# Performance work log

Measured on AMD Instinct MI355X. Metric: run time of the kernel, lower is better.

The kernel has to match this reference:

```python
import jax, jax.numpy as jnp
import numpy as np

B, S, D = 1, 2048, 1024
H, HD = 16, 64            # attn_num, head dim (D = H*HD)
TE, K, ED = 16, 2, 512    # experts, top_k, expert_dim
DS = 2048                 # shared_expert_dim
EPS = 1e-5
THETA = 10000.0
RSF = 1.0                 # routed_scaling_factor


def rmsnorm(x, w):
    return x * jax.lax.rsqrt(jnp.mean(x * x, axis=-1, keepdims=True) + EPS) * w


def rope(x):
    # x: [B,H,S,a]; half-split rotary as in RotaryEmb
    a = x.shape[-1]
    inv = (1.0 / THETA) ** (jnp.arange(0, a, 2, dtype=jnp.float32) / a)
    fr = jnp.outer(jnp.arange(x.shape[2], dtype=jnp.float32), inv)[None, None]  # [1,1,S,a/2]
    c, s = jnp.cos(fr), jnp.sin(fr)
    x1, x2 = jnp.split(x, 2, axis=-1)
    return jnp.concatenate([x1 * c + x2 * s, -x1 * s + x2 * c], axis=-1)


def setup_inputs() -> dict:
    key = jax.random.key(0)
    ks = jax.random.split(key, 16)
    w = 0.02
    return {
        "x_input": jax.random.normal(ks[0], (B, S, D), jnp.float32),
        "indices": jax.random.randint(ks[1], (B * S, K), 0, TE),
        "values": jax.random.normal(ks[2], (B * S, K), jnp.float32),
        "attn_w": jax.random.normal(ks[3], (3 * D, D), jnp.float32) * w,
        "attn_o_w": jax.random.normal(ks[4], (D, D), jnp.float32) * w,
        "attn_norm_w": jnp.ones((D,), jnp.float32),
        "ffn_norm_w": jnp.ones((D,), jnp.float32),
        "ffn_experts": jax.random.normal(ks[5], (3, TE, D, ED), jnp.float32) * w,
        "main_keys": jax.random.normal(ks[6], (D, TE), jnp.float32) * w,
        "main_bias": jnp.zeros((TE,), jnp.float32),
        "output_coeff": jnp.ones((1, 1, D), jnp.float32),
        "ffn_up_w": jax.random.normal(ks[7], (2 * DS, D), jnp.float32) * w,
        "ffn_down_w": jax.random.normal(ks[8], (D, DS), jnp.float32) * w,
        "shared_norm_w": jnp.ones((D,), jnp.float32),
    }


def reference(x_input, indices, values, attn_w, attn_o_w, attn_norm_w, ffn_norm_w,
              ffn_experts, main_keys, main_bias, output_coeff, ffn_up_w,
              ffn_down_w, shared_norm_w):
    # --- attention block ---
    x = rmsnorm(x_input, attn_norm_w)
    qkv = x @ attn_w.T                                  # [B,S,3D]
    xq, xk, xv = jnp.split(qkv, 3, axis=-1)
    def heads(t):
        return t.reshape(B, S, H, HD).transpose(0, 2, 1, 3)  # [B,H,S,HD]
    q, k, v = rope(heads(xq)), rope(heads(xk)), heads(xv)
    att = jnp.einsum('bhqa,bhka->bhqk', q, k) / jnp.sqrt(jnp.float32(HD))
    causal = jnp.tril(jnp.ones((S, S), bool))
    att = jnp.where(causal, att, jnp.finfo(att.dtype).min)
    att = jax.nn.softmax(att, axis=-1)
    o = jnp.einsum('bhqk,bhka->bhqa', att, v)
    x_attn = o.transpose(0, 2, 1, 3).reshape(B, S, D)
    x_ffn_input = x_attn @ attn_o_w.T + x_input

    # --- router ---
    x_ffn = rmsnorm(x_ffn_input, ffn_norm_w)
    T = B * S
    token_values = (x_ffn @ main_keys).reshape(T, TE)
    tv = jnp.take_along_axis(token_values, indices, axis=-1)  # [T,K]
    vals = values + tv + main_bias[indices]
    scores = jax.nn.softmax(vals, axis=-1) * RSF              # [T,K]

    # --- grouped GEMM experts (SwiGLU), dense combine over experts ---
    combine = jnp.zeros((T, TE), x_ffn.dtype).at[
        jnp.arange(T)[:, None], indices].add(scores)          # [T,TE]
    xf = x_ffn.reshape(T, D)
    h1 = jnp.einsum('td,edh->eth', xf, ffn_experts[0])
    h2 = jnp.einsum('td,edh->eth', xf, ffn_experts[1])
    g = jax.nn.silu(h1) * h2                                  # [TE,T,ED]
    ye = jnp.einsum('eth,edh->etd', g, ffn_experts[2])        # [TE,T,D]
    y = jnp.einsum('etd,te->td', ye, combine).reshape(B, S, D)
    y = y * output_coeff

    # --- shared SwiGLU expert ---
    x1, x2 = jnp.split(x_ffn @ ffn_up_w.T, 2, axis=-1)
    y_shared = (jax.nn.silu(x1) * x2) @ ffn_down_w.T
    y_shared = rmsnorm(y_shared, shared_norm_w)

    return y + y_shared + x_ffn_input
```

## Files before the change

kernel.cpp:

```cpp
#include <hip/hip_runtime.h>
#include <hip/hip_bf16.h>

using bf16 = __hip_bfloat16;

#define S_   2048
#define D_   1024
#define H_   16
#define HD_  64
#define TE_  16
#define ED_  512
#define DS_  2048
#define CAP_ 512

#define NEG_ -1e30f

typedef __attribute__((ext_vector_type(8))) short bf16x8;
typedef __attribute__((ext_vector_type(4))) short bf16x4;
typedef __attribute__((ext_vector_type(4))) float f32x4;
#define MFMA16(a, b, c) __builtin_amdgcn_mfma_f32_16x16x32_bf16(a, b, c, 0, 0, 0)

__device__ __forceinline__ void storeF(float* p, float v) { *p = v; }
__device__ __forceinline__ void storeF(bf16* p, float v)  { *p = __float2bfloat16(v); }
__device__ __forceinline__ short cvt1(float f) {
    bf16 h = __float2bfloat16(f);
    return *(short*)&h;
}
__device__ __forceinline__ float b2f(short s) {
    return __uint_as_float(((unsigned)(unsigned short)s) << 16);
}

__device__ __forceinline__ void load16(const bf16* g, short* l) {
    __builtin_amdgcn_global_load_lds(
        (const __attribute__((address_space(1))) unsigned*)g,
        (__attribute__((address_space(3))) unsigned*)l, 16, 0, 0);
}

__global__ __launch_bounds__(256) void convert_kernel(
        const float* __restrict__ src, bf16* __restrict__ dst)
{
    const size_t i = ((size_t)blockIdx.x*256 + threadIdx.x)*8;
    const float4 f0 = *(const float4*)(src + i);
    const float4 f1 = *(const float4*)(src + i + 4);
    short t8[8];
    t8[0]=cvt1(f0.x); t8[1]=cvt1(f0.y); t8[2]=cvt1(f0.z); t8[3]=cvt1(f0.w);
    t8[4]=cvt1(f1.x); t8[5]=cvt1(f1.y); t8[6]=cvt1(f1.z); t8[7]=cvt1(f1.w);
    *(bf16x8*)(dst + i) = *(bf16x8*)t8;
}

__global__ __launch_bounds__(256) void mkT_kernel(
        const float* __restrict__ mk, float* __restrict__ mkT)
{
    const int idx = blockIdx.x*256 + threadIdx.x;
    const int e = idx >> 10, d = idx & 1023;
    mkT[idx] = mk[d*TE_ + e];
}

__global__ __launch_bounds__(256) void rmsnorm_kernel(
        const float* __restrict__ x, const float* __restrict__ w,
        bf16* __restrict__ out)
{
    const int t = blockIdx.x, tid = threadIdx.x;
    __shared__ float red[4];
    const float4 xv = *(const float4*)(x + (size_t)t*D_ + tid*4);
    float ss = xv.x*xv.x + xv.y*xv.y + xv.z*xv.z + xv.w*xv.w;
#pragma unroll
    for (int off = 32; off; off >>= 1) ss += __shfl_xor(ss, off, 64);
    if ((tid & 63) == 0) red[tid >> 6] = ss;
    __syncthreads();
    const float rn = rsqrtf((red[0]+red[1]+red[2]+red[3]) * (1.f/D_) + 1e-5f);
    const float4 wv = *(const float4*)(w + tid*4);
    short o[4];
    o[0] = cvt1(xv.x*rn*wv.x); o[1] = cvt1(xv.y*rn*wv.y);
    o[2] = cvt1(xv.z*rn*wv.z); o[3] = cvt1(xv.w*rn*wv.w);
    *(bf16x4*)(out + (size_t)t*D_ + tid*4) = *(bf16x4*)o;
}

template<typename OutT, bool HAS_RES>
__global__ __launch_bounds__(256) void gemm_mfma_bb_kernel(
    const bf16* __restrict__ A, const bf16* __restrict__ B,
    OutT* __restrict__ C, const float* __restrict__ Res,
    int M, int N, int K)
{
    __shared__ short As[2][128*32];
    __shared__ short Bs[2][128*32];
    const int tid = threadIdx.x;
    const int w = tid >> 6, l = tid & 63;
    const int wm = w >> 1, wn = w & 1;
    const int m0 = blockIdx.y * 128, n0 = blockIdx.x * 128;
    const int lr = l >> 2, lq = l & 3;
    const int fm = l & 15, fq = l >> 4;
    f32x4 acc[4][4];
#pragma unroll
    for (int i = 0; i < 4; ++i)
#pragma unroll
        for (int j = 0; j < 4; ++j) acc[i][j] = (f32x4){0.f,0.f,0.f,0.f};

    const bf16* ga = A + (size_t)(m0 + w*16 + lr)*K + lq*8;
    const bf16* gb = B + (size_t)(n0 + w*16 + lr)*K + lq*8;
    load16(ga,                &As[0][(w*16)*32]);
    load16(ga + (size_t)64*K, &As[0][(64 + w*16)*32]);
    load16(gb,                &Bs[0][(w*16)*32]);
    load16(gb + (size_t)64*K, &Bs[0][(64 + w*16)*32]);
    __syncthreads();
    const int nk = K >> 5;
    for (int t = 0; t < nk; ++t) {
        const int cur = t & 1;
        if (t + 1 < nk) {
            const int k1 = (t + 1) << 5;
            load16(ga + k1,                &As[cur^1][(w*16)*32]);
            load16(ga + k1 + (size_t)64*K, &As[cur^1][(64 + w*16)*32]);
            load16(gb + k1,                &Bs[cur^1][(w*16)*32]);
            load16(gb + k1 + (size_t)64*K, &Bs[cur^1][(64 + w*16)*32]);
        }
        bf16x8 af[4], bfr[4];
#pragma unroll
        for (int mi = 0; mi < 4; ++mi)
            af[mi] = *(const bf16x8*)&As[cur][(wm*64 + mi*16 + fm)*32 + fq*8];
#pragma unroll
        for (int ni = 0; ni < 4; ++ni)
            bfr[ni] = *(const bf16x8*)&Bs[cur][(wn*64 + ni*16 + fm)*32 + fq*8];
#pragma unroll
        for (int mi = 0; mi < 4; ++mi)
#pragma unroll
            for (int ni = 0; ni < 4; ++ni)
                acc[mi][ni] = MFMA16(af[mi], bfr[ni], acc[mi][ni]);
        __syncthreads();
    }
#pragma unroll
    for (int mi = 0; mi < 4; ++mi)
#pragma unroll
        for (int ni = 0; ni < 4; ++ni)
#pragma unroll
            for (int r = 0; r < 4; ++r) {
                const int row = m0 + wm*64 + mi*16 + fq*4 + r;
                const int col = n0 + wn*64 + ni*16 + fm;
                float v = acc[mi][ni][r];
                if constexpr (HAS_RES) v += Res[(size_t)row*N + col];
                storeF(&C[(size_t)row*N + col], v);
            }
}

__global__ __launch_bounds__(256) void transpose_kernel(
    const float* __restrict__ src, bf16* __restrict__ dst)
{
    __shared__ bf16 tile[64][65];
    const int h0 = blockIdx.x*64, d0 = blockIdx.y*64, m = blockIdx.z;
    const float* s = src + (size_t)m*D_*ED_;
    bf16*        o = dst + (size_t)m*ED_*D_;
    const int tid = threadIdx.x;
#pragma unroll
    for (int i = 0; i < 16; ++i) {
        const int idx = tid + 256*i;
        const int r = idx >> 6, c = idx & 63;
        tile[r][c] = __float2bfloat16(s[(size_t)(d0 + r)*ED_ + h0 + c]);
    }
    __syncthreads();
#pragma unroll
    for (int i = 0; i < 16; ++i) {
        const int idx = tid + 256*i;
        const int r = idx >> 6, c = idx & 63;
        o[(size_t)(h0 + r)*D_ + d0 + c] = tile[c][r];
    }
}

__global__ __launch_bounds__(256) void expert_mid_mfma_kernel(
    const bf16* __restrict__ xffn, const bf16* __restrict__ w0t,
    const int* __restrict__ counts, const int* __restrict__ pairs,
    const float* __restrict__ pw, bf16* __restrict__ gbuf)
{
    const int ht = blockIdx.x, pt = blockIdx.y, e = blockIdx.z;
    const int cnt = counts[e];
    if (pt*128 >= cnt) return;
    __shared__ short Xs[2][128*32];
    __shared__ short W0s[2][64*32];
    __shared__ short W1s[2][64*32];
    __shared__ int   toks[128];
    __shared__ float wrow[128];
    const int tid = threadIdx.x;
    const int w = tid >> 6, l = tid & 63;
    const int wm = w >> 1, wn = w & 1;
    const int lr = l >> 2, lq = l & 3;
    const int fm = l & 15, fq = l >> 4;
    if (tid < 128) {
        const int p = pt*128 + tid;
        if (p < cnt) { toks[tid] = pairs[e*CAP_ + p] >> 1; wrow[tid] = pw[e*CAP_ + p]; }
        else         { toks[tid] = 0;                      wrow[tid] = 0.f; }
    }
    __syncthreads();
    const int t0 = toks[w*16 + lr], t1 = toks[64 + w*16 + lr];
    const bf16* gx0 = xffn + (size_t)t0*D_ + lq*8;
    const bf16* gx1 = xffn + (size_t)t1*D_ + lq*8;
    const bf16* g0  = w0t + ((size_t)e*ED_ + ht*64 + w*16 + lr)*D_ + lq*8;
    const bf16* g1  = w0t + ((size_t)(16 + e)*ED_ + ht*64 + w*16 + lr)*D_ + lq*8;
    f32x4 acc1[4][2], acc2[4][2];
#pragma unroll
    for (int i = 0; i < 4; ++i)
#pragma unroll
        for (int j = 0; j < 2; ++j) {
            acc1[i][j] = (f32x4){0.f,0.f,0.f,0.f};
            acc2[i][j] = (f32x4){0.f,0.f,0.f,0.f};
        }
    load16(gx0, &Xs[0][(w*16)*32]);
    load16(gx1, &Xs[0][(64 + w*16)*32]);
    load16(g0,  &W0s[0][(w*16)*32]);
    load16(g1,  &W1s[0][(w*16)*32]);
    __syncthreads();
    const int nk = D_ >> 5;
    for (int t = 0; t < nk; ++t) {
        const int cur = t & 1;
        if (t + 1 < nk) {
            const int k1 = (t + 1) << 5;
            load16(gx0 + k1, &Xs[cur^1][(w*16)*32]);
            load16(gx1 + k1, &Xs[cur^1][(64 + w*16)*32]);
            load16(g0 + k1,  &W0s[cur^1][(w*16)*32]);
            load16(g1 + k1,  &W1s[cur^1][(w*16)*32]);
        }
        bf16x8 af[4], b0[2], b1[2];
#pragma unroll
        for (int mi = 0; mi < 4; ++mi)
            af[mi] = *(const bf16x8*)&Xs[cur][(wm*64 + mi*16 + fm)*32 + fq*8];
#pragma unroll
        for (int ni = 0; ni < 2; ++ni) {
            b0[ni] = *(const bf16x8*)&W0s[cur][(wn*32 + ni*16 + fm)*32 + fq*8];
            b1[ni] = *(const bf16x8*)&W1s[cur][(wn*32 + ni*16 + fm)*32 + fq*8];
        }
#pragma unroll
        for (int mi = 0; mi < 4; ++mi)
#pragma unroll
            for (int ni = 0; ni < 2; ++ni) {
                acc1[mi][ni] = MFMA16(af[mi], b0[ni], acc1[mi][ni]);
                acc2[mi][ni] = MFMA16(af[mi], b1[ni], acc2[mi][ni]);
            }
        __syncthreads();
    }
#pragma unroll
    for (int mi = 0; mi < 4; ++mi)
#pragma unroll
        for (int ni = 0; ni < 2; ++ni)
#pragma unroll
            for (int r = 0; r < 4; ++r) {
                const int row = wm*64 + mi*16 + fq*4 + r;
                const int col = wn*32 + ni*16 + fm;
                const float h1 = acc1[mi][ni][r], h2 = acc2[mi][ni][r];
                const float g = wrow[row] * (h1 / (1.f + __expf(-h1))) * h2;
                gbuf[((size_t)e*CAP_ + pt*128 + row)*ED_ + ht*64 + col] = __float2bfloat16(g);
            }
}

__global__ __launch_bounds__(256) void expert_down_mfma_kernel(
    const bf16* __restrict__ gbuf, const bf16* __restrict__ w2,
    const int* __restrict__ counts, const int* __restrict__ pairs,
    bf16* __restrict__ ytk)
{
    const int nt = blockIdx.x, pt = blockIdx.y, e = blockIdx.z;
    const int cnt = counts[e];
    if (pt*128 >= cnt) return;
    __shared__ short As[2][128*32];
    __shared__ short Bs[2][128*32];
    __shared__ int prs[128];
    const int tid = threadIdx.x;
    const int w = tid >> 6, l = tid & 63;
    const int wm = w >> 1, wn = w & 1;
    const int lr = l >> 2, lq = l & 3;
    const int fm = l & 15, fq = l >> 4;
    if (tid < 128) {
        const int p = pt*128 + tid;
        prs[tid] = (p < cnt) ? pairs[e*CAP_ + p] : -1;
    }
    __syncthreads();
    const bf16* ga = gbuf + ((size_t)e*CAP_ + pt*128 + w*16 + lr)*ED_ + lq*8;
    const bf16* gb = w2 + (size_t)e*D_*ED_ + (size_t)(nt*128 + w*16 + lr)*ED_ + lq*8;
    f32x4 acc[4][4];
#pragma unroll
    for (int i = 0; i < 4; ++i)
#pragma unroll
        for (int j = 0; j < 4; ++j) acc[i][j] = (f32x4){0.f,0.f,0.f,0.f};
    load16(ga,                  &As[0][(w*16)*32]);
    load16(ga + (size_t)64*ED_, &As[0][(64 + w*16)*32]);
    load16(gb,                  &Bs[0][(w*16)*32]);
    load16(gb + (size_t)64*ED_, &Bs[0][(64 + w*16)*32]);
    __syncthreads();
    const int nk = ED_ >> 5;
    for (int t = 0; t < nk; ++t) {
        const int cur = t & 1;
        if (t + 1 < nk) {
            const int k1 = (t + 1) << 5;
            load16(ga + k1,                  &As[cur^1][(w*16)*32]);
            load16(ga + k1 + (size_t)64*ED_, &As[cur^1][(64 + w*16)*32]);
            load16(gb + k1,                  &Bs[cur^1][(w*16)*32]);
            load16(gb + k1 + (size_t)64*ED_, &Bs[cur^1][(64 + w*16)*32]);
        }
        bf16x8 af[4], bfr[4];
#pragma unroll
        for (int mi = 0; mi < 4; ++mi)
            af[mi] = *(const bf16x8*)&As[cur][(wm*64 + mi*16 + fm)*32 + fq*8];
#pragma unroll
        for (int ni = 0; ni < 4; ++ni)
            bfr[ni] = *(const bf16x8*)&Bs[cur][(wn*64 + ni*16 + fm)*32 + fq*8];
#pragma unroll
        for (int mi = 0; mi < 4; ++mi)
#pragma unroll
            for (int ni = 0; ni < 4; ++ni)
                acc[mi][ni] = MFMA16(af[mi], bfr[ni], acc[mi][ni]);
        __syncthreads();
    }
#pragma unroll
    for (int mi = 0; mi < 4; ++mi)
#pragma unroll
        for (int r = 0; r < 4; ++r) {
            const int pr = prs[wm*64 + mi*16 + fq*4 + r];
            if (pr < 0) continue;
#pragma unroll
            for (int ni = 0; ni < 4; ++ni) {
                const int col = nt*128 + wn*64 + ni*16 + fm;
                ytk[(size_t)pr*D_ + col] = __float2bfloat16(acc[mi][ni][r]);
            }
        }
}

__global__ __launch_bounds__(256) void rope_kernel(const bf16* __restrict__ qkv,
        bf16* __restrict__ qr, bf16* __restrict__ kswz)
{
    const int s = blockIdx.x, tid = threadIdx.x;
    const int c = s & 63, jt = s >> 6;
    for (int it = tid; it < 512; it += 256) {
        const int h = it >> 5, i = it & 31;
        const float inv = exp2f(-(float)i * 0.41524101186091903f);
        const float fr = (float)s * inv;
        float sn, cs;
        sincosf(fr, &sn, &cs);
        const size_t qb = (size_t)s*3072 + h*64 + i;
        const float q1 = __bfloat162float(qkv[qb]);
        const float q2 = __bfloat162float(qkv[qb + 32]);
        const size_t ob = ((size_t)h*S_ + s)*64 + i;
        qr[ob]      = __float2bfloat16(0.125f*( q1*cs + q2*sn));
        qr[ob + 32] = __float2bfloat16(0.125f*(-q1*sn + q2*cs));
        const float k1 = __bfloat162float(qkv[qb + 1024]);
        const float k2 = __bfloat162float(qkv[qb + 1024 + 32]);
        const size_t kb = ((size_t)(h*32 + jt))*4096 + (size_t)c*64;
        const int j0 = (i >> 3) ^ (c & 7);
        const int j1 = (4 + (i >> 3)) ^ (c & 7);
        kswz[kb + j0*8 + (i & 7)] = __float2bfloat16( k1*cs + k2*sn);
        kswz[kb + j1*8 + (i & 7)] = __float2bfloat16(-k1*sn + k2*cs);
    }
}

__global__ __launch_bounds__(256) void vtrans_kernel(
    const bf16* __restrict__ qkv, bf16* __restrict__ vswz)
{
    const int jt = blockIdx.x, h = blockIdx.y;
    __shared__ short Vt[64][72];
    const int tid = threadIdx.x;
#pragma unroll
    for (int it = 0; it < 2; ++it) {
        const int idx = it*256 + tid;
        const int cc = idx >> 3, seg = idx & 7;
        *(bf16x8*)&Vt[cc][seg*8] =
            *(const bf16x8*)(qkv + (size_t)(jt*64 + cc)*3072 + 2048 + h*64 + seg*8);
    }
    __syncthreads();
    bf16* out = vswz + ((size_t)(h*32 + jt))*4096;
#pragma unroll
    for (int it = 0; it < 2; ++it) {
        const int q = it*256 + tid;
        const int a = q >> 3, jo = q & 7;
        const int j = jo ^ (a & 7);
        short t8[8];
#pragma unroll
        for (int e = 0; e < 8; ++e) t8[e] = Vt[j*8 + e][a];
        *(bf16x8*)(out + a*64 + jo*8) = *(bf16x8*)t8;
    }
}

__global__ __launch_bounds__(512) void attn_mfma_kernel(
    const bf16* __restrict__ qr, const bf16* __restrict__ kswz,
    const bf16* __restrict__ vswz, bf16* __restrict__ xattn)
{
    const int p = blockIdx.x, h = blockIdx.y;
    __shared__ short Ks[2][2][4096];
    __shared__ short Vs[2][2][4096];
    __shared__ short Ps[2][64][72];
    __shared__ float Oc[64][64];
    __shared__ float Mc[64], Lc[64];
    const int tid = threadIdx.x;
    const int w = tid >> 6, l = tid & 63;
    const int g = w >> 2, gw = w & 3;
    const int fm = l & 15, fq = l >> 4;
    const int sr = gw * 16;
    const bf16* ktile = kswz + (size_t)h*32*4096;
    const bf16* vtile = vswz + (size_t)h*32*4096;

    auto stageKV = [&](int jtile, int bufidx) {
        const bf16* ks_ = ktile + (size_t)jtile*4096 + gw*1024 + l*8;
        const bf16* vs_ = vtile + (size_t)jtile*4096 + gw*1024 + l*8;
        short* kd_ = &Ks[g][bufidx][gw*1024];
        short* vd_ = &Vs[g][bufidx][gw*1024];
        load16(ks_,       kd_);
        load16(ks_ + 512, kd_ + 512);
        load16(vs_,       vd_);
        load16(vs_ + 512, vd_ + 512);
    };

    for (int half = 0; half < 2; ++half) {
        const int qt = half ? (31 - p) : p;
        const bf16* gq = qr + ((size_t)h*S_ + qt*64 + sr + fm)*64 + fq*8;
        const bf16x8 aq0 = *(const bf16x8*)gq;
        const bf16x8 aq1 = *(const bf16x8*)(gq + 32);
        f32x4 Oa[4];
        float m_i[4], l_i[4];
#pragma unroll
        for (int i = 0; i < 4; ++i) {
            Oa[i] = (f32x4){0.f,0.f,0.f,0.f};
            m_i[i] = NEG_; l_i[i] = 0.f;
        }
        const int nj = qt + 1;
        const int itmax = (nj + 1) >> 1;
        if (g < nj) stageKV(g, 0);
        __syncthreads();
        for (int it = 0; it < itmax; ++it) {
            const int jt = g + 2*it;
            const int buf = it & 1;
            if (jt + 2 < nj) stageKV(jt + 2, buf ^ 1);
            if (jt < nj) {
                const short* kb = &Ks[g][buf][0];
                const short* vb = &Vs[g][buf][0];
                f32x4 sc[4];
#pragma unroll
                for (int ni = 0; ni < 4; ++ni) sc[ni] = (f32x4){0.f,0.f,0.f,0.f};
                __builtin_amdgcn_s_setprio(1);
#pragma unroll
                for (int ni = 0; ni < 4; ++ni) {
                    const int row = ni*16 + fm;
                    bf16x8 bk0 = *(const bf16x8*)&kb[row*64 + (( fq      ^ (fm & 7))<<3)];
                    bf16x8 bk1 = *(const bf16x8*)&kb[row*64 + (((fq + 4) ^ (fm & 7))<<3)];
                    sc[ni] = MFMA16(aq0, bk0, sc[ni]);
                    sc[ni] = MFMA16(aq1, bk1, sc[ni]);
                }
                __builtin_amdgcn_s_setprio(0);
                const bool diag = (jt == qt);
#pragma unroll
                for (int r = 0; r < 4; ++r) {
                    const int rowin = sr + fq*4 + r;
                    float rm = NEG_;
#pragma unroll
                    for (int ni = 0; ni < 4; ++ni) {
                        if (diag && (ni*16 + fm) > rowin) sc[ni][r] = NEG_;
                        rm = fmaxf(rm, sc[ni][r]);
                    }
                    rm = fmaxf(rm, __shfl_xor(rm, 1, 16));
                    rm = fmaxf(rm, __shfl_xor(rm, 2, 16));
                    rm = fmaxf(rm, __shfl_xor(rm, 4, 16));
                    rm = fmaxf(rm, __shfl_xor(rm, 8, 16));
                    const float mnew  = fmaxf(m_i[r], rm);
                    const float alpha = __expf(m_i[r] - mnew);
                    float rs = 0.f;
#pragma unroll
                    for (int ni = 0; ni < 4; ++ni) {
                        const float pv = __expf(sc[ni][r] - mnew);
                        sc[ni][r] = pv; rs += pv;
                    }
                    rs += __shfl_xor(rs, 1, 16);
                    rs += __shfl_xor(rs, 2, 16);
                    rs += __shfl_xor(rs, 4, 16);
                    rs += __shfl_xor(rs, 8, 16);
                    l_i[r] = l_i[r]*alpha + rs;
                    m_i[r] = mnew;
#pragma unroll
                    for (int ni = 0; ni < 4; ++ni) Oa[ni][r] *= alpha;
                }
#pragma unroll
                for (int ni = 0; ni < 4; ++ni)
#pragma unroll
                    for (int r = 0; r < 4; ++r)
                        Ps[g][sr + fq*4 + r][ni*16 + fm] = cvt1(sc[ni][r]);
                bf16x8 ap0 = *(const bf16x8*)&Ps[g][sr + fm][fq*8];
                bf16x8 ap1 = *(const bf16x8*)&Ps[g][sr + fm][32 + fq*8];
                __builtin_amdgcn_s_setprio(1);
#pragma unroll
                for (int ni = 0; ni < 4; ++ni) {
                    const int row = ni*16 + fm;
                    bf16x8 bv0 = *(const bf16x8*)&vb[row*64 + (( fq      ^ (fm & 7))<<3)];
                    bf16x8 bv1 = *(const bf16x8*)&vb[row*64 + (((fq + 4) ^ (fm & 7))<<3)];
                    Oa[ni] = MFMA16(ap0, bv0, Oa[ni]);
                    Oa[ni] = MFMA16(ap1, bv1, Oa[ni]);
                }
                __builtin_amdgcn_s_setprio(0);
            }
            __syncthreads();
        }
        if (g == 1) {
#pragma unroll
            for (int r = 0; r < 4; ++r) {
                const int row = sr + fq*4 + r;
                if (fm == 0) { Mc[row] = m_i[r]; Lc[row] = l_i[r]; }
#pragma unroll
                for (int ni = 0; ni < 4; ++ni) Oc[row][ni*16 + fm] = Oa[ni][r];
            }
        }
        __syncthreads();
        if (g == 0) {
#pragma unroll
            for (int r = 0; r < 4; ++r) {
                const int row = sr + fq*4 + r;
                const float m1 = Mc[row], l1 = Lc[row];
                const float mm = fmaxf(m_i[r], m1);
                const float a0 = __expf(m_i[r] - mm), a1 = __expf(m1 - mm);
                const float inv = 1.f / (l_i[r]*a0 + l1*a1);
                const int srow = qt*64 + row;
#pragma unroll
                for (int ni = 0; ni < 4; ++ni)
                    xattn[(size_t)srow*D_ + h*64 + ni*16 + fm] =
                        __float2bfloat16((Oa[ni][r]*a0 + Oc[row][ni*16 + fm]*a1)*inv);
            }
        }
        __syncthreads();
    }
}

__global__ __launch_bounds__(256) void router_kernel(
    const bf16* __restrict__ xffn, const int* __restrict__ indices,
    const float* __restrict__ values, const float* __restrict__ mkT,
    const float* __restrict__ mbias, int* __restrict__ counts,
    int* __restrict__ pairs, float* __restrict__ pw)
{
    const int wv = threadIdx.x >> 6, lane = threadIdx.x & 63;
    const int t = blockIdx.x*4 + wv;
    const int i0 = indices[t*2], i1 = indices[t*2 + 1];
    const bf16* xp = xffn + (size_t)t*D_ + lane*16;
    const bf16x8 xa = *(const bf16x8*)xp;
    const bf16x8 xb = *(const bf16x8*)(xp + 8);
    float xv[16];
#pragma unroll
    for (int j = 0; j < 8; ++j) { xv[j] = b2f(xa[j]); xv[8 + j] = b2f(xb[j]); }
    const float* k0 = mkT + (size_t)i0*D_ + lane*16;
    const float* k1 = mkT + (size_t)i1*D_ + lane*16;
    float a0[16], a1[16];
#pragma unroll
    for (int j = 0; j < 4; ++j) {
        *(float4*)&a0[j*4] = *(const float4*)(k0 + j*4);
        *(float4*)&a1[j*4] = *(const float4*)(k1 + j*4);
    }
    float s0 = 0.f, s1 = 0.f;
#pragma unroll
    for (int j = 0; j < 16; ++j) {
        s0 = fmaf(xv[j], a0[j], s0);
        s1 = fmaf(xv[j], a1[j], s1);
    }
#pragma unroll
    for (int off = 32; off; off >>= 1) {
        s0 += __shfl_xor(s0, off, 64);
        s1 += __shfl_xor(s1, off, 64);
    }
    if (lane == 0) {
        const float v0 = values[t*2]     + s0 + mbias[i0];
        const float v1 = values[t*2 + 1] + s1 + mbias[i1];
        const float mx = fmaxf(v0, v1);
        const float e0 = __expf(v0 - mx), e1 = __expf(v1 - mx);
        const float inv = 1.f / (e0 + e1);
        const int p0 = atomicAdd(&counts[i0], 1);
        if (p0 < CAP_) { pairs[i0*CAP_ + p0] = t*2;     pw[i0*CAP_ + p0] = e0*inv; }
        const int p1 = atomicAdd(&counts[i1], 1);
        if (p1 < CAP_) { pairs[i1*CAP_ + p1] = t*2 + 1; pw[i1*CAP_ + p1] = e1*inv; }
    }
}

__global__ __launch_bounds__(256) void silu_mul_kernel(const bf16* __restrict__ u,
        bf16* __restrict__ gsh)
{
    const int idx = blockIdx.x*256 + threadIdx.x;
    const int t = idx >> 8, j = idx & 255;
    const bf16x8 av = *(const bf16x8*)(u + (size_t)t*(2*DS_) + j*8);
    const bf16x8 bv = *(const bf16x8*)(u + (size_t)t*(2*DS_) + DS_ + j*8);
    short o[8];
#pragma unroll
    for (int k = 0; k < 8; ++k) {
        const float a = b2f(av[k]), b = b2f(bv[k]);
        o[k] = cvt1(a / (1.f + __expf(-a)) * b);
    }
    *(bf16x8*)(gsh + (size_t)idx*8) = *(bf16x8*)o;
}

__global__ __launch_bounds__(256) void final_kernel(
    const bf16* __restrict__ ytk, const float* __restrict__ ysh,
    const float* __restrict__ xffin, const float* __restrict__ coeff,
    const float* __restrict__ shw, float* __restrict__ out)
{
    const int t = blockIdx.x, tid = threadIdx.x;
    __shared__ float red[4];
    const float4 yv = *(const float4*)(ysh + (size_t)t*D_ + tid*4);
    float ss = yv.x*yv.x + yv.y*yv.y + yv.z*yv.z + yv.w*yv.w;
#pragma unroll
    for (int off = 32; off; off >>= 1) ss += __shfl_xor(ss, off, 64);
    if ((tid & 63) == 0) red[tid >> 6] = ss;
    __syncthreads();
    const float rn = rsqrtf((red[0]+red[1]+red[2]+red[3]) * (1.f/D_) + 1e-5f);
    const int d = tid*4;
    const bf16x4 y0 = *(const bf16x4*)(ytk + (size_t)(t*2)*D_ + d);
    const bf16x4 y1 = *(const bf16x4*)(ytk + (size_t)(t*2 + 1)*D_ + d);
    const float4 cf = *(const float4*)(coeff + d);
    const float4 sw = *(const float4*)(shw + d);
    const float4 xf = *(const float4*)(xffin + (size_t)t*D_ + d);
    float4 o;
    o.x = (b2f(y0[0]) + b2f(y1[0]))*cf.x + yv.x*rn*sw.x + xf.x;
    o.y = (b2f(y0[1]) + b2f(y1[1]))*cf.y + yv.y*rn*sw.y + xf.y;
    o.z = (b2f(y0[2]) + b2f(y1[2]))*cf.z + yv.z*rn*sw.z + xf.z;
    o.w = (b2f(y0[3]) + b2f(y1[3]))*cf.w + yv.w*rn*sw.w + xf.w;
    *(float4*)(out + (size_t)t*D_ + d) = o;
}

extern "C" void kernel_launch(void* const* d_in, const int* in_sizes, int n_in,
                              void* d_out, int out_size, void* d_ws, size_t ws_size,
                              hipStream_t stream)
{
    const float* x_input     = (const float*)d_in[0];
    const int*   indices     = (const int*)  d_in[1];
    const float* values      = (const float*)d_in[2];
    const float* attn_w      = (const float*)d_in[3];
    const float* attn_o_w    = (const float*)d_in[4];
    const float* attn_norm_w = (const float*)d_in[5];
    const float* ffn_norm_w  = (const float*)d_in[6];
    const float* ffn_experts = (const float*)d_in[7];
    const float* main_keys   = (const float*)d_in[8];
    const float* main_bias   = (const float*)d_in[9];
    const float* out_coeff   = (const float*)d_in[10];
    const float* ffn_up_w    = (const float*)d_in[11];
    const float* ffn_down_w  = (const float*)d_in[12];
    const float* shared_nw   = (const float*)d_in[13];

    char* wp = (char*)d_ws;
    auto alloc = [&](size_t n) { char* p = wp; wp += (n + 255) & ~(size_t)255; return p; };
    char*  regA   = alloc(28*1024*1024 + 4096);
    bf16*  xn     = (bf16*)(regA);
    bf16*  qkv    = (bf16*)(regA + 4*1024*1024);
    bf16*  qr     = (bf16*)(regA + 16*1024*1024);
    bf16*  xattn  = (bf16*)(regA + 20*1024*1024);
    bf16*  w2bf   = (bf16*)(regA);
    bf16*  u      = (bf16*)(regA);
    bf16*  gsh    = (bf16*)(regA + 16*1024*1024);
    float* xffin  = (float*)alloc((size_t)S_*D_*4);
    bf16*  kswz   = (bf16*)xffin;
    bf16*  vswz   = kswz + (size_t)H_*32*4096;
    bf16*  xffn   = (bf16*) alloc((size_t)S_*D_*2);
    int*   counts = (int*)  alloc(TE_*4);
    int*   pairs  = (int*)  alloc((size_t)TE_*CAP_*4);
    float* pwgt   = (float*)alloc((size_t)TE_*CAP_*4);
    float* mkT    = (float*)alloc((size_t)TE_*D_*4);
    bf16*  gbuf   = (bf16*) alloc((size_t)TE_*CAP_*ED_*2);
    bf16*  o_bf   = (bf16*)gbuf;
    float* ysh    = (float*)((char*)gbuf);
    bf16*  ytk    = (bf16*) alloc((size_t)S_*2*D_*2);
    bf16*  awbf   = (bf16*)ytk;
    bf16*  w0t    = (bf16*) alloc((size_t)2*TE_*ED_*D_*2);
    bf16*  upbf   = (bf16*)w0t;
    bf16*  dnbf   = (bf16*)((char*)w0t + 8*1024*1024);

    hipMemsetAsync(counts, 0, TE_*4, stream);

    transpose_kernel<<<dim3(ED_/64, D_/64, 2*TE_), 256, 0, stream>>>(ffn_experts, w0t);
    convert_kernel<<<(3*D_*D_)/2048, 256, 0, stream>>>(attn_w, awbf);
    convert_kernel<<<(D_*D_)/2048, 256, 0, stream>>>(attn_o_w, o_bf);
    mkT_kernel<<<(TE_*D_)/256, 256, 0, stream>>>(main_keys, mkT);

    rmsnorm_kernel<<<S_, 256, 0, stream>>>(x_input, attn_norm_w, xn);
    gemm_mfma_bb_kernel<bf16,false><<<dim3(3*D_/128, S_/128), 256, 0, stream>>>(
        xn, awbf, qkv, nullptr, S_, 3*D_, D_);
    rope_kernel<<<S_, 256, 0, stream>>>(qkv, qr, kswz);
    vtrans_kernel<<<dim3(S_/64, H_), 256, 0, stream>>>(qkv, vswz);
    convert_kernel<<<(TE_*D_*ED_)/2048, 256, 0, stream>>>(
        ffn_experts + (size_t)2*TE_*D_*ED_, w2bf);
    attn_mfma_kernel<<<dim3(16, H_), 512, 0, stream>>>(qr, kswz, vswz, xattn);
    gemm_mfma_bb_kernel<float,true><<<dim3(D_/128, S_/128), 256, 0, stream>>>(
        xattn, o_bf, xffin, x_input, S_, D_, D_);

    rmsnorm_kernel<<<S_, 256, 0, stream>>>(xffin, ffn_norm_w, xffn);
    router_kernel<<<S_/4, 256, 0, stream>>>(xffn, indices, values, mkT, main_bias,
                                            counts, pairs, pwgt);
    expert_mid_mfma_kernel<<<dim3(ED_/64, CAP_/128, TE_), 256, 0, stream>>>(
        xffn, w0t, counts, pairs, pwgt, gbuf);
    convert_kernel<<<(2*DS_*D_)/2048, 256, 0, stream>>>(ffn_up_w, upbf);
    convert_kernel<<<(D_*DS_)/2048, 256, 0, stream>>>(ffn_down_w, dnbf);
    expert_down_mfma_kernel<<<dim3(D_/128, CAP_/128, TE_), 256, 0, stream>>>(
        gbuf, w2bf, counts, pairs, ytk);

    gemm_mfma_bb_kernel<bf16,false><<<dim3(2*DS_/128, S_/128), 256, 0, stream>>>(
        xffn, upbf, u, nullptr, S_, 2*DS_, D_);
    silu_mul_kernel<<<(S_*DS_)/2048, 256, 0, stream>>>(u, gsh);
    gemm_mfma_bb_kernel<float,false><<<dim3(D_/128, S_/128), 256, 0, stream>>>(
        gsh, dnbf, ysh, nullptr, S_, D_, DS_);

    final_kernel<<<S_, 256, 0, stream>>>(ytk, ysh, xffin, out_coeff, shared_nw,
                                         (float*)d_out);
}
```

Before: 509.5 us.

## Add narrow-N GEMM tile variant, block swizzle, and reorder weight conversions

The GEMM kernel takes a BN template parameter. N=1024 GEMMs (attention output and shared down projection) now use a 128x64 tile, which doubles the block count from 128 to 256 so the MI355X's many CUs are better filled. A block-index swizzle groups consecutive blocks for L2 reuse. The expert weight transpose and conversion launches are moved later in the stream, likely to fit buffer aliasing or ordering. The risks are less reuse per block on the smaller tiles and correctness hazards from the reordering, since the buffers are aliased.

```diff
diff --git a/kernel.cpp b/kernel.cpp
--- a/kernel.cpp
+++ b/kernel.cpp
@@ -75,23 +75,29 @@
     *(bf16x4*)(out + (size_t)t*D_ + tid*4) = *(bf16x4*)o;
 }
 
-template<typename OutT, bool HAS_RES>
+template<typename OutT, bool HAS_RES, int BN>
 __global__ __launch_bounds__(256) void gemm_mfma_bb_kernel(
     const bf16* __restrict__ A, const bf16* __restrict__ B,
     OutT* __restrict__ C, const float* __restrict__ Res,
     int M, int N, int K)
 {
+    constexpr int MI = (BN == 128) ? 4 : 2;
     __shared__ short As[2][128*32];
-    __shared__ short Bs[2][128*32];
+    __shared__ short Bs[2][BN*32];
     const int tid = threadIdx.x;
     const int w = tid >> 6, l = tid & 63;
-    const int wm = w >> 1, wn = w & 1;
-    const int m0 = blockIdx.y * 128, n0 = blockIdx.x * 128;
+    const int wm = (BN == 128) ? (w >> 1) : w;
+    const int wn = (BN == 128) ? (w & 1) : 0;
+    const int nwg = gridDim.x * gridDim.y;
+    const int bid = blockIdx.y * gridDim.x + blockIdx.x;
+    const int swz = ((nwg & 7) == 0) ? ((bid & 7) * (nwg >> 3) + (bid >> 3)) : bid;
+    const int bx = swz % gridDim.x, by = swz / gridDim.x;
+    const int m0 = by * 128, n0 = bx * BN;
     const int lr = l >> 2, lq = l & 3;
     const int fm = l & 15, fq = l >> 4;
-    f32x4 acc[4][4];
-#pragma unroll
-    for (int i = 0; i < 4; ++i)
+    f32x4 acc[MI][4];
+#pragma unroll
+    for (int i = 0; i < MI; ++i)
 #pragma unroll
         for (int j = 0; j < 4; ++j) acc[i][j] = (f32x4){0.f,0.f,0.f,0.f};
 
@@ -100,7 +106,8 @@
     load16(ga,                &As[0][(w*16)*32]);
     load16(ga + (size_t)64*K, &As[0][(64 + w*16)*32]);
     load16(gb,                &Bs[0][(w*16)*32]);
-    load16(gb + (size_t)64*K, &Bs[0][(64 + w*16)*32]);
+    if constexpr (BN == 128)
+        load16(gb + (size_t)64*K, &Bs[0][(64 + w*16)*32]);
     __syncthreads();
     const int nk = K >> 5;
     for (int t = 0; t < nk; ++t) {
@@ -110,29 +117,30 @@
             load16(ga + k1,                &As[cur^1][(w*16)*32]);
             load16(ga + k1 + (size_t)64*K, &As[cur^1][(64 + w*16)*32]);
             load16(gb + k1,                &Bs[cur^1][(w*16)*32]);
-            load16(gb + k1 + (size_t)64*K, &Bs[cur^1][(64 + w*16)*32]);
-        }
-        bf16x8 af[4], bfr[4];
-#pragma unroll
-        for (int mi = 0; mi < 4; ++mi)
-            af[mi] = *(const bf16x8*)&As[cur][(wm*64 + mi*16 + fm)*32 + fq*8];
+            if constexpr (BN == 128)
+                load16(gb + k1 + (size_t)64*K, &Bs[cur^1][(64 + w*16)*32]);
+        }
+        bf16x8 af[MI], bfr[4];
+#pragma unroll
+        for (int mi = 0; mi < MI; ++mi)
+            af[mi] = *(const bf16x8*)&As[cur][(wm*(MI*16) + mi*16 + fm)*32 + fq*8];
 #pragma unroll
         for (int ni = 0; ni < 4; ++ni)
             bfr[ni] = *(const bf16x8*)&Bs[cur][(wn*64 + ni*16 + fm)*32 + fq*8];
 #pragma unroll
-        for (int mi = 0; mi < 4; ++mi)
+        for (int mi = 0; mi < MI; ++mi)
 #pragma unroll
             for (int ni = 0; ni < 4; ++ni)
                 acc[mi][ni] = MFMA16(af[mi], bfr[ni], acc[mi][ni]);
         __syncthreads();
     }
 #pragma unroll
-    for (int mi = 0; mi < 4; ++mi)
+    for (int mi = 0; mi < MI; ++mi)
 #pragma unroll
         for (int ni = 0; ni < 4; ++ni)
 #pragma unroll
             for (int r = 0; r < 4; ++r) {
-                const int row = m0 + wm*64 + mi*16 + fq*4 + r;
+                const int row = m0 + wm*(MI*16) + mi*16 + fq*4 + r;
                 const int col = n0 + wn*64 + ni*16 + fm;
                 float v = acc[mi][ni][r];
                 if constexpr (HAS_RES) v += Res[(size_t)row*N + col];
@@ -656,25 +664,27 @@
 
     hipMemsetAsync(counts, 0, TE_*4, stream);
 
-    transpose_kernel<<<dim3(ED_/64, D_/64, 2*TE_), 256, 0, stream>>>(ffn_experts, w0t);
     convert_kernel<<<(3*D_*D_)/2048, 256, 0, stream>>>(attn_w, awbf);
     convert_kernel<<<(D_*D_)/2048, 256, 0, stream>>>(attn_o_w, o_bf);
     mkT_kernel<<<(TE_*D_)/256, 256, 0, stream>>>(main_keys, mkT);
 
     rmsnorm_kernel<<<S_, 256, 0, stream>>>(x_input, attn_norm_w, xn);
-    gemm_mfma_bb_kernel<bf16,false><<<dim3(3*D_/128, S_/128), 256, 0, stream>>>(
+    gemm_mfma_bb_kernel<bf16,false,128><<<dim3(3*D_/128, S_/128), 256, 0, stream>>>(
         xn, awbf, qkv, nullptr, S_, 3*D_, D_);
     rope_kernel<<<S_, 256, 0, stream>>>(qkv, qr, kswz);
     vtrans_kernel<<<dim3(S_/64, H_), 256, 0, stream>>>(qkv, vswz);
-    convert_kernel<<<(TE_*D_*ED_)/2048, 256, 0, stream>>>(
-        ffn_experts + (size_t)2*TE_*D_*ED_, w2bf);
     attn_mfma_kernel<<<dim3(16, H_), 512, 0, stream>>>(qr, kswz, vswz, xattn);
-    gemm_mfma_bb_kernel<float,true><<<dim3(D_/128, S_/128), 256, 0, stream>>>(
+
+    transpose_kernel<<<dim3(ED_/64, D_/64, 2*TE_), 256, 0, stream>>>(ffn_experts, w0t);
+
+    gemm_mfma_bb_kernel<float,true,64><<<dim3(D_/64, S_/128), 256, 0, stream>>>(
         xattn, o_bf, xffin, x_input, S_, D_, D_);
 
     rmsnorm_kernel<<<S_, 256, 0, stream>>>(xffin, ffn_norm_w, xffn);
     router_kernel<<<S_/4, 256, 0, stream>>>(xffn, indices, values, mkT, main_bias,
                                             counts, pairs, pwgt);
+    convert_kernel<<<(TE_*D_*ED_)/2048, 256, 0, stream>>>(
+        ffn_experts + (size_t)2*TE_*D_*ED_, w2bf);
     expert_mid_mfma_kernel<<<dim3(ED_/64, CAP_/128, TE_), 256, 0, stream>>>(
         xffn, w0t, counts, pairs, pwgt, gbuf);
     convert_kernel<<<(2*DS_*D_)/2048, 256, 0, stream>>>(ffn_up_w, upbf);
@@ -682,10 +692,10 @@
     expert_down_mfma_kernel<<<dim3(D_/128, CAP_/128, TE_), 256, 0, stream>>>(
         gbuf, w2bf, counts, pairs, ytk);
 
-    gemm_mfma_bb_kernel<bf16,false><<<dim3(2*DS_/128, S_/128), 256, 0, stream>>>(
+    gemm_mfma_bb_kernel<bf16,false,128><<<dim3(2*DS_/128, S_/128), 256, 0, stream>>>(
         xffn, upbf, u, nullptr, S_, 2*DS_, D_);
     silu_mul_kernel<<<(S_*DS_)/2048, 256, 0, stream>>>(u, gsh);
-    gemm_mfma_bb_kernel<float,false><<<dim3(D_/128, S_/128), 256, 0, stream>>>(
+    gemm_mfma_bb_kernel<float,false,64><<<dim3(D_/64, S_/128), 256, 0, stream>>>(
         gsh, dnbf, ysh, nullptr, S_, D_, DS_);
 
     final_kernel<<<S_, 256, 0, stream>>>(ytk, ysh, xffin, out_coeff, shared_nw,
```

After: 494.3 us. 3.0% less time.
